# Kernel optimization log

Hardware: AMD Instinct MI355X
Metric: run time of the kernel (lower is better)

The kernel has to match this reference:

```python
import jax, jax.numpy as jnp
import numpy as np
from jax import lax

DN = ('NCDHW', 'OIDHW', 'NCDHW')

def conv3d(x, w, b, stride, pad):
    y = lax.conv_general_dilated(x, w, (stride,) * 3, [(pad, pad)] * 3,
                                 dimension_numbers=DN)
    return y + b[None, :, None, None, None]

def conv_transpose3d(x, w, b, stride=2, pad=1):
    # torch ConvTranspose3d weight layout: (Cin, Cout, k, k, k).
    # Equivalent conv: flip spatial dims, swap in/out, lhs_dilation=stride,
    # padding = k - 1 - pad.
    k = w.shape[2]
    wf = jnp.flip(w, (2, 3, 4)).transpose(1, 0, 2, 3, 4)
    p = k - 1 - pad
    y = lax.conv_general_dilated(x, wf, (1, 1, 1), [(p, p)] * 3,
                                 lhs_dilation=(stride,) * 3,
                                 dimension_numbers=DN)
    return y + b[None, :, None, None, None]

def setup_inputs() -> dict:
    key = jax.random.key(0)
    ks = jax.random.split(key, 20)
    B, C, S = 2, 3, 64
    CD, K = 256, 1024  # codebook_dim, codebook_size

    def w(k, shape):
        fan_in = int(np.prod(shape[1:]))
        return (jax.random.normal(k, shape, jnp.float32) / np.sqrt(fan_in)).astype(jnp.float32)

    inp = {"x": jax.random.normal(ks[0], (B, C, S, S, S), jnp.float32)}
    # encoder
    inp["enc_w1"] = w(ks[1], (64, C, 4, 4, 4));   inp["enc_b1"] = jnp.zeros((64,), jnp.float32)
    inp["enc_w2"] = w(ks[2], (128, 64, 4, 4, 4)); inp["enc_b2"] = jnp.zeros((128,), jnp.float32)
    inp["enc_w3"] = w(ks[3], (256, 128, 4, 4, 4)); inp["enc_b3"] = jnp.zeros((256,), jnp.float32)
    inp["enc_w4"] = w(ks[4], (CD, 256, 1, 1, 1)); inp["enc_b4"] = jnp.zeros((CD,), jnp.float32)
    # codebook (nn.Embedding weight)
    inp["codebook"] = jax.random.normal(ks[5], (K, CD), jnp.float32)
    # decoder (ConvTranspose weights in torch (Cin, Cout, k, k, k) layout)
    inp["dec_w1"] = w(ks[6], (CD, 256, 4, 4, 4)); inp["dec_b1"] = jnp.zeros((256,), jnp.float32)
    inp["dec_w2"] = w(ks[7], (256, 128, 4, 4, 4)); inp["dec_b2"] = jnp.zeros((128,), jnp.float32)
    inp["dec_w3"] = w(ks[8], (128, 64, 4, 4, 4)); inp["dec_b3"] = jnp.zeros((64,), jnp.float32)
    inp["dec_w4"] = w(ks[9], (C, 64, 4, 4, 4));   inp["dec_b4"] = jnp.zeros((C,), jnp.float32)
    return inp

def reference(x, enc_w1, enc_b1, enc_w2, enc_b2, enc_w3, enc_b3, enc_w4, enc_b4,
              codebook, dec_w1, dec_b1, dec_w2, dec_b2, dec_w3, dec_b3, dec_w4, dec_b4):
    # encoder
    h = jax.nn.relu(conv3d(x, enc_w1, enc_b1, 2, 1))
    h = jax.nn.relu(conv3d(h, enc_w2, enc_b2, 2, 1))
    h = jax.nn.relu(conv3d(h, enc_w3, enc_b3, 2, 1))
    latent = conv3d(h, enc_w4, enc_b4, 1, 0)  # (B, CD, H, W, D)
    B = latent.shape[0]
    H, W, D = latent.shape[2], latent.shape[3], latent.shape[4]
    CD = codebook.shape[1]
    # Faithful to torch: raw row-major .view(B, -1, CD) on channel-first latent
    lat = latent.reshape(B, -1, CD)  # (B, N, CD), N = H*W*D
    # argmin of L2 norm == argmin of squared distance (expand-norm trick,
    # avoids materializing the (B,N,K,CD) broadcast tensor)
    d2 = ((lat * lat).sum(-1, keepdims=True)
          - 2.0 * jnp.einsum('bnd,kd->bnk', lat, codebook)
          + (codebook * codebook).sum(-1)[None, None, :])  # (B, N, K)
    quantized_idx = jnp.argmin(d2, axis=-1)  # (B, N)
    quantized = codebook[quantized_idx]      # (B, N, CD)
    q = quantized.reshape(B, H, W, D, CD).transpose(0, 4, 1, 2, 3)  # (B, CD, H, W, D)
    # decoder
    h = jax.nn.relu(conv_transpose3d(q, dec_w1, dec_b1))
    h = jax.nn.relu(conv_transpose3d(h, dec_w2, dec_b2))
    h = jax.nn.relu(conv_transpose3d(h, dec_w3, dec_b3))
    reconstructed = jnp.tanh(conv3d(h, dec_w4, dec_b4, 1, 0))  # (B, C, S-3, S-3, S-3)
    return reconstructed, quantized_idx
```

## Files before the change

### kernel.cpp

```cpp
#include <hip/hip_runtime.h>
#include <cfloat>
#include <cmath>


using f32x4  = __attribute__((ext_vector_type(4))) float;
using bf16x8 = __attribute__((ext_vector_type(8))) short;
typedef float f32x4u __attribute__((ext_vector_type(4), aligned(4)));
typedef unsigned short u16x4u __attribute__((ext_vector_type(4), aligned(4)));
typedef unsigned short u16x8a4 __attribute__((ext_vector_type(8), aligned(4)));

__device__ __forceinline__ unsigned short f32_to_bf16(float f) {
    unsigned int u = __float_as_uint(f);
    u += 0x7fffu + ((u >> 16) & 1u);
    return (unsigned short)(u >> 16);
}
__device__ __forceinline__ void split_bf16(float v, unsigned short& h, unsigned short& l) {
    h = f32_to_bf16(v);
    float hf = __uint_as_float((unsigned)h << 16);
    l = f32_to_bf16(v - hf);
}
struct bf16t { unsigned short u; };
__device__ __forceinline__ void store_act(float* p, float v) { *p = v; }
__device__ __forceinline__ void store_act(unsigned short* p, float v) { *p = f32_to_bf16(v); }
__device__ __forceinline__ void store_act(bf16t* p, float v) {
    p->u = (unsigned short)(__float_as_uint(v) >> 16);
}

template <typename V>
__device__ __forceinline__ bf16x8 pack_b(V r0, V r1) {
    bf16x8 b;
    b[0] = (short)r0[0]; b[1] = (short)r0[1]; b[2] = (short)r0[2]; b[3] = (short)r0[3];
    b[4] = (short)r1[0]; b[5] = (short)r1[1]; b[6] = (short)r1[2]; b[7] = (short)r1[3];
    return b;
}

__global__ __launch_bounds__(256)
void prep_split_w(const float* __restrict__ w, short* __restrict__ whi,
                  short* __restrict__ wlo, long total)
{
    long idx = (long)blockIdx.x * blockDim.x + threadIdx.x;
    if (idx >= total) return;
    unsigned short h, l;
    split_bf16(w[idx], h, l);
    whi[idx] = (short)h; wlo[idx] = (short)l;
}

__global__ __launch_bounds__(256)
void prep_split_w_frag(const float* __restrict__ w, short* __restrict__ whi,
                       short* __restrict__ wlo, int CIN, int COUT)
{
    const int K = CIN * 64;
    const int MT = COUT >> 4;
    long total = (long)COUT * K;
    long idx = (long)blockIdx.x * blockDim.x + threadIdx.x;
    if (idx >= total) return;
    int kk = (int)(idx & 7); long r = idx >> 3;
    int l  = (int)(r & 63);  r >>= 6;
    int m  = (int)(r % MT);
    int s  = (int)(r / MT);
    int n16 = l & 15, quad = l >> 4;
    int co = m * 16 + n16;
    int korig = s * 32 + quad * 8 + kk;
    unsigned short h, lo16;
    split_bf16(w[(long)co * K + korig], h, lo16);
    whi[idx] = (short)h; wlo[idx] = (short)lo16;
}

__global__ __launch_bounds__(256)
void pad_input_split(const float* __restrict__ x, unsigned short* __restrict__ xhi,
                     unsigned short* __restrict__ xlo)
{
    const int D = 64, PD = 66, PRX = 68, BC = 6;
    long total = (long)BC * PD * PD * PRX;
    long idx = (long)blockIdx.x * blockDim.x + threadIdx.x;
    if (idx >= total) return;
    int px = (int)(idx % PRX); long t = idx / PRX;
    int py = (int)(t % PD); t /= PD;
    int pz = (int)(t % PD); int c = (int)(t / PD);
    int ix = px - 1, iy = py - 1, iz = pz - 1;
    float v = 0.0f;
    if ((unsigned)ix < (unsigned)D && (unsigned)iy < (unsigned)D && (unsigned)iz < (unsigned)D)
        v = x[(((long)c * D + iz) * D + iy) * D + ix];
    unsigned short h, l;
    split_bf16(v, h, l);
    xhi[idx] = h; xlo[idx] = l;
}

__global__ __launch_bounds__(256)
void zero_halo_ps(unsigned short* __restrict__ p, int C, int PD, int PRX)
{
    long total = (long)C * PD * PD * PRX;
    long idx = (long)blockIdx.x * blockDim.x + threadIdx.x;
    if (idx >= total) return;
    int px = (int)(idx % PRX); long t = idx / PRX;
    int py = (int)(t % PD); t /= PD;
    int pz = (int)(t % PD);
    if (px == 0 || px >= PD - 1 || py == 0 || py == PD - 1 || pz == 0 || pz == PD - 1)
        p[idx] = 0;
}

template <typename T>
__global__ __launch_bounds__(256) void zero_halo_t(T* __restrict__ p, int C, int PD)
{
    long total = (long)C * PD * PD * PD;
    long idx = (long)blockIdx.x * blockDim.x + threadIdx.x;
    if (idx >= total) return;
    int px = (int)(idx % PD); long t = idx / PD;
    int py = (int)(t % PD); t /= PD;
    int pz = (int)(t % PD);
    if (px == 0 || px == PD - 1 || py == 0 || py == PD - 1 || pz == 0 || pz == PD - 1)
        p[idx] = (T)0;
}

template <int CIN, int COUT, int DOUT, int PD, int PRX, int MTW, int OWT,
          int OWHALF, int KSPLIT, int OUTSPLIT>
__global__ __launch_bounds__(256)
void conv_s2_mfma(const unsigned short* __restrict__ xhi,
                  const unsigned short* __restrict__ xlo,
                  const short* __restrict__ Whi, const short* __restrict__ Wlo,
                  const float* __restrict__ bias,
                  unsigned short* __restrict__ yhi, unsigned short* __restrict__ ylo,
                  float* __restrict__ yf,
                  int OPD, int OPRX, int po, long sstride)
{
    constexpr int K = CIN * 64;
    constexpr int MWAVES = COUT / (16 * MTW);
    constexpr int RPB = 4 / MWAVES;
    constexpr int KN = (CIN * 2) / KSPLIT;

    int bx = blockIdx.x;
    const int ks = (KSPLIT > 1) ? (bx % KSPLIT) : 0;
    const int rowblk = (KSPLIT > 1) ? (bx / KSPLIT) : bx;
    const int lane = (int)threadIdx.x & 63, w = (int)threadIdx.x >> 6;
    const int mi = (MWAVES == 4) ? w : 0;
    const int ri = (MWAVES == 4) ? 0 : w;
    const int rowid = rowblk * RPB + ri;
    const int n16 = lane & 15, quad = lane >> 4;

    int b, od, oh, ow;
    if (OWHALF) {
        constexpr int NOH = DOUT / 2;
        const int ohb = rowid % NOH; int t = rowid / NOH;
        od = t % DOUT; b = t / DOUT;
        oh = ohb * 2 + (n16 >> 3);
        ow = n16 & 7;
    } else {
        const int owt = rowid % OWT; int t = rowid / OWT;
        oh = t % DOUT; t /= DOUT;
        od = t % DOUT; b = t / DOUT;
        ow = owt * 16 + n16;
    }

    const int co0 = mi * (MTW * 16);

    f32x4 acc[MTW];
    #pragma unroll
    for (int mt = 0; mt < MTW; ++mt)
        #pragma unroll
        for (int r = 0; r < 4; ++r) {
            int co = co0 + mt * 16 + quad * 4 + r;
            acc[mt][r] = (ks == 0) ? bias[co] : 0.0f;
        }

    const int sg0 = ks * KN;
    const long chs = (long)PD * PD * PRX;
    long off = ((long)(b * CIN + (sg0 >> 1)) * PD + (2 * od + (quad >> 1))) * PD * PRX
             + (long)(2 * oh + (quad & 1) * 2) * PRX + 2 * ow;
    const unsigned short* phi = xhi + off;
    const unsigned short* plo = xlo + off;
    const long incA = 2L * PD * PRX;
    const long incB = chs - 2L * PD * PRX;

    const short* a0h = Whi + (long)(co0 + n16) * K + sg0 * 32 + quad * 8;
    const short* a0l = Wlo + (long)(co0 + n16) * K + sg0 * 32 + quad * 8;

    #pragma unroll 2
    for (int s = 0; s < KN; ++s) {
        u16x4u h0 = *(const u16x4u*)phi;
        u16x4u h1 = *(const u16x4u*)(phi + PRX);
        u16x4u l0 = *(const u16x4u*)plo;
        u16x4u l1 = *(const u16x4u*)(plo + PRX);
        bf16x8 bhi = pack_b(h0, h1);
        bf16x8 blo = pack_b(l0, l1);
        #pragma unroll
        for (int mt = 0; mt < MTW; ++mt) {
            bf16x8 ah = *(const bf16x8*)(a0h + (long)mt * 16 * K + s * 32);
            bf16x8 al = *(const bf16x8*)(a0l + (long)mt * 16 * K + s * 32);
            acc[mt] = __builtin_amdgcn_mfma_f32_16x16x32_bf16(ah, bhi, acc[mt], 0, 0, 0);
            acc[mt] = __builtin_amdgcn_mfma_f32_16x16x32_bf16(ah, blo, acc[mt], 0, 0, 0);
            acc[mt] = __builtin_amdgcn_mfma_f32_16x16x32_bf16(al, bhi, acc[mt], 0, 0, 0);
        }
        long inc = (s & 1) ? incB : incA;
        phi += inc; plo += inc;
    }

    if (OUTSPLIT) {
        #pragma unroll
        for (int mt = 0; mt < MTW; ++mt)
            #pragma unroll
            for (int r = 0; r < 4; ++r) {
                int co = co0 + mt * 16 + quad * 4 + r;
                float v = fmaxf(acc[mt][r], 0.0f);
                unsigned short h, l;
                split_bf16(v, h, l);
                long o = (((long)(b * COUT + co) * OPD + od + po) * OPD + oh + po) * OPRX
                       + ow + po;
                yhi[o] = h; ylo[o] = l;
            }
    } else {
        #pragma unroll
        for (int mt = 0; mt < MTW; ++mt)
            #pragma unroll
            for (int r = 0; r < 4; ++r) {
                int co = co0 + mt * 16 + quad * 4 + r;
                long o = (long)ks * sstride
                       + (((long)(b * COUT + co) * OPD + od) * OPD + oh) * OPRX + ow;
                yf[o] = acc[mt][r];
            }
    }
}

template <int CIN, int COUT, int DOUT, int PD, int PRX, int MTW, int OWT,
          int OWHALF, int KSPLIT, int OUTSPLIT>
__global__ __launch_bounds__(256)
void conv_s2_mfma_fd(const unsigned short* __restrict__ xhi,
                     const unsigned short* __restrict__ xlo,
                     const short* __restrict__ Whi, const short* __restrict__ Wlo,
                     const float* __restrict__ bias,
                     unsigned short* __restrict__ yhi, unsigned short* __restrict__ ylo,
                     float* __restrict__ yf,
                     int OPD, int OPRX, int po, long sstride)
{
    constexpr int MWAVES = COUT / (16 * MTW);
    constexpr int RPB = 4 / MWAVES;
    constexpr int KN = (CIN * 2) / KSPLIT;
    constexpr int MT = COUT >> 4;
    constexpr int SSTEP = MT * 512;

    int bx = blockIdx.x;
    const int ks = (KSPLIT > 1) ? (bx % KSPLIT) : 0;
    const int rowblk = (KSPLIT > 1) ? (bx / KSPLIT) : bx;
    const int lane = (int)threadIdx.x & 63, w = (int)threadIdx.x >> 6;
    const int mi = (MWAVES == 4) ? w : 0;
    const int ri = (MWAVES == 4) ? 0 : w;
    const int rowid = rowblk * RPB + ri;
    const int n16 = lane & 15, quad = lane >> 4;

    int b, od, oh, ow;
    if (OWHALF) {
        constexpr int NOH = DOUT / 2;
        const int ohb = rowid % NOH; int t = rowid / NOH;
        od = t % DOUT; b = t / DOUT;
        oh = ohb * 2 + (n16 >> 3);
        ow = n16 & 7;
    } else {
        const int owt = rowid % OWT; int t = rowid / OWT;
        oh = t % DOUT; t /= DOUT;
        od = t % DOUT; b = t / DOUT;
        ow = owt * 16 + n16;
    }

    const int co0 = mi * (MTW * 16);

    f32x4 acc[MTW];
    #pragma unroll
    for (int mt = 0; mt < MTW; ++mt)
        #pragma unroll
        for (int r = 0; r < 4; ++r) {
            int co = co0 + mt * 16 + quad * 4 + r;
            acc[mt][r] = (ks == 0) ? bias[co] : 0.0f;
        }

    const int sg0 = ks * KN;
    const long chs = (long)PD * PD * PRX;
    long off = ((long)(b * CIN + (sg0 >> 1)) * PD + (2 * od + (quad >> 1))) * PD * PRX
             + (long)(2 * oh + (quad & 1) * 2) * PRX + 2 * ow;
    const unsigned short* phi = xhi + off;
    const unsigned short* plo = xlo + off;
    const long incA = 2L * PD * PRX;
    const long incB = chs - 2L * PD * PRX;

    const short* ph = Whi + (((long)sg0 * MT + mi * MTW) * 64 + lane) * 8;
    const short* pl = Wlo + (((long)sg0 * MT + mi * MTW) * 64 + lane) * 8;

    #pragma unroll 2
    for (int s = 0; s < KN; ++s) {
        u16x4u h0 = *(const u16x4u*)phi;
        u16x4u h1 = *(const u16x4u*)(phi + PRX);
        u16x4u l0 = *(const u16x4u*)plo;
        u16x4u l1 = *(const u16x4u*)(plo + PRX);
        bf16x8 bhi = pack_b(h0, h1);
        bf16x8 blo = pack_b(l0, l1);
        #pragma unroll
        for (int mt = 0; mt < MTW; ++mt) {
            bf16x8 ah = *(const bf16x8*)(ph + mt * 512);
            bf16x8 al = *(const bf16x8*)(pl + mt * 512);
            acc[mt] = __builtin_amdgcn_mfma_f32_16x16x32_bf16(ah, bhi, acc[mt], 0, 0, 0);
            acc[mt] = __builtin_amdgcn_mfma_f32_16x16x32_bf16(ah, blo, acc[mt], 0, 0, 0);
            acc[mt] = __builtin_amdgcn_mfma_f32_16x16x32_bf16(al, bhi, acc[mt], 0, 0, 0);
        }
        long inc = (s & 1) ? incB : incA;
        phi += inc; plo += inc;
        ph += SSTEP; pl += SSTEP;
    }

    if (OUTSPLIT) {
        #pragma unroll
        for (int mt = 0; mt < MTW; ++mt)
            #pragma unroll
            for (int r = 0; r < 4; ++r) {
                int co = co0 + mt * 16 + quad * 4 + r;
                float v = fmaxf(acc[mt][r], 0.0f);
                unsigned short h, l;
                split_bf16(v, h, l);
                long o = (((long)(b * COUT + co) * OPD + od + po) * OPD + oh + po) * OPRX
                       + ow + po;
                yhi[o] = h; ylo[o] = l;
            }
    } else {
        #pragma unroll
        for (int mt = 0; mt < MTW; ++mt)
            #pragma unroll
            for (int r = 0; r < 4; ++r) {
                int co = co0 + mt * 16 + quad * 4 + r;
                long o = (long)ks * sstride
                       + (((long)(b * COUT + co) * OPD + od) * OPD + oh) * OPRX + ow;
                yf[o] = acc[mt][r];
            }
    }
}

__global__ __launch_bounds__(256)
void combine4_relu(const float* __restrict__ p, float* __restrict__ y, long N, long ss)
{
    long idx = (long)blockIdx.x * blockDim.x + threadIdx.x;
    if (idx >= N) return;
    float v = p[idx] + p[idx + ss] + p[idx + 2 * ss] + p[idx + 3 * ss];
    y[idx] = fmaxf(v, 0.0f);
}

__global__ __launch_bounds__(128)
void conv1x1_b(const float* __restrict__ x, const float* __restrict__ w,
               const float* __restrict__ bias, float* __restrict__ y)
{
    const int co = blockIdx.x & 255, b = blockIdx.x >> 8;
    const int s4 = (int)threadIdx.x * 4;
    const float* xb = x + (long)b * 256 * 512 + s4;
    const float* wr = w + (long)co * 256;
    float bv = bias[co];
    float4 acc = {bv, bv, bv, bv};
    for (int ci = 0; ci < 256; ++ci) {
        float wv = wr[ci];
        float4 xv = *(const float4*)(xb + (long)ci * 512);
        acc.x = fmaf(xv.x, wv, acc.x); acc.y = fmaf(xv.y, wv, acc.y);
        acc.z = fmaf(xv.z, wv, acc.z); acc.w = fmaf(xv.w, wv, acc.w);
    }
    *(float4*)(y + (long)(b * 256 + co) * 512 + s4) = acc;
}

__global__ void codenorm_kernel(const float* __restrict__ cb, float* __restrict__ norms)
{
    int k = blockIdx.x;
    int lane = threadIdx.x;
    float s = 0.0f;
    const float* row = cb + (long)k * 256;
    for (int d = lane; d < 256; d += 64) { float v = row[d]; s = fmaf(v, v, s); }
    for (int off = 32; off > 0; off >>= 1) s += __shfl_down(s, off);
    if (lane == 0) norms[k] = s;
}

__global__ __launch_bounds__(256)
void transpose_cb(const float* __restrict__ cb, float* __restrict__ cbT)
{
    int idx = blockIdx.x * 256 + (int)threadIdx.x;
    int d = idx & 255, k = idx >> 8;
    cbT[(long)d * 1024 + k] = cb[(long)k * 256 + d];
}

__global__ __launch_bounds__(256)
void vq_kernel4(const float* __restrict__ lat, const float* __restrict__ cb,
                const float* __restrict__ cbT, const float* __restrict__ norms,
                unsigned short* __restrict__ q, float* __restrict__ idx_out)
{
    __shared__ __align__(16) float rows[4][256];
    __shared__ float s_best[4][256];
    __shared__ int   s_bidx[4][256];
    const int r0 = blockIdx.x * 4;
    const int t = (int)threadIdx.x;

    #pragma unroll
    for (int j = 0; j < 4; ++j)
        rows[j][t] = lat[(long)(r0 + j) * 256 + t];
    __syncthreads();

    float latn[4];
    #pragma unroll
    for (int j = 0; j < 4; ++j) {
        const float4* rowv = (const float4*)rows[j];
        float a = 0.0f;
        #pragma unroll 4
        for (int d = 0; d < 64; ++d) {
            float4 rv = rowv[d];
            a = fmaf(rv.x, rv.x, a); a = fmaf(rv.y, rv.y, a);
            a = fmaf(rv.z, rv.z, a); a = fmaf(rv.w, rv.w, a);
        }
        latn[j] = a;
    }

    float dot[4][4] = {};
    const float* ct = cbT + t * 4;
    #pragma unroll 4
    for (int d = 0; d < 256; ++d) {
        float4 c4 = *(const float4*)(ct + (long)d * 1024);
        #pragma unroll
        for (int j = 0; j < 4; ++j) {
            float rv = rows[j][d];
            dot[j][0] = fmaf(rv, c4.x, dot[j][0]);
            dot[j][1] = fmaf(rv, c4.y, dot[j][1]);
            dot[j][2] = fmaf(rv, c4.z, dot[j][2]);
            dot[j][3] = fmaf(rv, c4.w, dot[j][3]);
        }
    }

    float4 nv = *(const float4*)(norms + t * 4);
    float nr[4] = {nv.x, nv.y, nv.z, nv.w};

    #pragma unroll
    for (int j = 0; j < 4; ++j) {
        float best = FLT_MAX;
        int bidx = 0x7fffffff;
        #pragma unroll
        for (int c = 0; c < 4; ++c) {
            float sc = latn[j] - 2.0f * dot[j][c] + nr[c];
            int k = t * 4 + c;
            if (sc < best || (sc == best && k < bidx)) { best = sc; bidx = k; }
        }
        s_best[j][t] = best; s_bidx[j][t] = bidx;
    }
    __syncthreads();
    for (int off = 128; off > 0; off >>= 1) {
        if (t < off) {
            #pragma unroll
            for (int j = 0; j < 4; ++j) {
                float o = s_best[j][t + off]; int oi = s_bidx[j][t + off];
                if (o < s_best[j][t] || (o == s_best[j][t] && oi < s_bidx[j][t])) {
                    s_best[j][t] = o; s_bidx[j][t] = oi;
                }
            }
        }
        __syncthreads();
    }

    #pragma unroll
    for (int j = 0; j < 4; ++j) {
        const int bk = s_bidx[j][0];
        const int r = r0 + j;
        const int b = r >> 9, n = r & 511;
        const int zz = n >> 6, yy = (n >> 3) & 7, xx = n & 7;
        q[(long)(b * 256 + t) * 1000 + ((long)(zz + 1) * 10 + (yy + 1)) * 10 + (xx + 1)]
            = f32_to_bf16(cb[(long)bk * 256 + t]);
    }
    if (t == 0) {
        #pragma unroll
        for (int j = 0; j < 4; ++j)
            idx_out[r0 + j] = (float)s_bidx[j][0];
    }
}

__global__ __launch_bounds__(256)
void prep_convt_w(const float* __restrict__ w, short* __restrict__ Ap,
                  int Cin, int Cout, int xflip)
{
    const int K = Cin * 8;
    long total = 8L * Cout * K;
    long idx = (long)blockIdx.x * blockDim.x + threadIdx.x;
    if (idx >= total) return;
    int k = (int)(idx % K);
    int co = (int)((idx / K) % Cout);
    int p = (int)(idx / ((long)K * Cout));
    int ci = k >> 3, a = k & 7;
    int az = (a >> 2) & 1, ay = (a >> 1) & 1, ax = a & 1;
    int pz = p >> 2, py = (p >> 1) & 1, px = p & 1;
    int axw = xflip ? (1 - ax) : ax;
    int kd = (1 - pz) + 2 * az, kh = (1 - py) + 2 * ay, kw = (1 - px) + 2 * axw;
    float v = w[((long)ci * Cout + co) * 64 + kd * 16 + kh * 4 + kw];
    Ap[idx] = (short)f32_to_bf16(v);
}

__global__ __launch_bounds__(256)
void prep_convt_w_frag(const float* __restrict__ w, short* __restrict__ Ap,
                       int Cin, int Cout, int xflip)
{
    const int MG = Cout >> 6;
    const int nsteps = Cin >> 2;
    long total = 8L * MG * nsteps * 2048;
    long idx = (long)blockIdx.x * blockDim.x + threadIdx.x;
    if (idx >= total) return;
    int kk = (int)(idx & 7); long r = idx >> 3;
    int l  = (int)(r & 63);  r >>= 6;
    int cb = (int)(r & 3);   r >>= 2;
    int s  = (int)(r % nsteps); r /= nsteps;
    int mg = (int)(r % MG);
    int p  = (int)(r / MG);

    int n16 = l & 15, quad = l >> 4;
    int korig = s * 32 + quad * 8 + kk;
    int co = mg * 64 + cb * 16 + n16;
    int ci = korig >> 3, a = korig & 7;
    int az = (a >> 2) & 1, ay = (a >> 1) & 1, ax = a & 1;
    int pz = p >> 2, py = (p >> 1) & 1, px = p & 1;
    int axw = xflip ? (1 - ax) : ax;
    int kd = (1 - pz) + 2 * az, kh = (1 - py) + 2 * ay, kw = (1 - px) + 2 * axw;
    float v = w[((long)ci * Cout + co) * 64 + kd * 16 + kh * 4 + kw];
    Ap[idx] = (short)f32_to_bf16(v);
}

template <int CIN, int COUT, int DIN, int OPAD, typename OutT>
__global__ __launch_bounds__(256)
void convt_mfma(const unsigned short* __restrict__ Xp, const short* __restrict__ Ap,
                const float* __restrict__ bias, OutT* __restrict__ Y)
{
    constexpr int PD = DIN + 2;
    constexpr int PD3 = PD * PD * PD;
    constexpr int T = DIN >> 2;
    constexpr int NT = T * T * T;
    constexpr int SLAB = NT / 8;
    constexpr int OPD = 2 * DIN + 2 * OPAD;
    constexpr int K = CIN * 8;
    constexpr int MG = COUT >> 6;
    constexpr int nsteps = K >> 5;

    int bx = blockIdx.x;
    const int xcd = bx & 7;
    int local = bx >> 3;
    const int px = local & 1; local >>= 1;
    const int mg = local % MG; local /= MG;
    const int ntin = local % SLAB;
    const int pzy = local / SLAB;
    const int pz = pzy >> 1, py = pzy & 1;
    const int p = pz * 4 + py * 2 + px;
    const int nt = xcd * SLAB + ntin;

    const int lane = threadIdx.x & 63, wave = threadIdx.x >> 6;
    const int n16 = lane & 15, quad = lane >> 4;

    const int tx = nt % T, ty = (nt / T) % T, tz = nt / (T * T);
    const int mz = tz * 4 + wave, my = ty * 4 + (n16 >> 2), mx = tx * 4 + (n16 & 3);
    const int sp = ((mz + pz) * PD + (my + py)) * PD + (mx + px);

    const unsigned short* xq = Xp + (long)quad * PD3 + sp;

    const int cobase = mg * 64;
    const short* ap0 = Ap + ((long)p * COUT + cobase + n16) * K + quad * 8;

    f32x4 acc[4];
    #pragma unroll
    for (int cb = 0; cb < 4; ++cb) {
        const float* bp = bias + cobase + cb * 16 + quad * 4;
        acc[cb][0] = bp[0]; acc[cb][1] = bp[1]; acc[cb][2] = bp[2]; acc[cb][3] = bp[3];
    }

    #pragma unroll 4
    for (int s = 0; s < nsteps; ++s) {
        const unsigned short* xs = xq + (long)s * 4 * PD3;
        bf16x8 bf;
        bf[0] = (short)xs[(PD + 1) * PD + 1];
        bf[1] = (short)xs[(PD + 1) * PD];
        bf[2] = (short)xs[PD * PD + 1];
        bf[3] = (short)xs[PD * PD];
        bf[4] = (short)xs[PD + 1];
        bf[5] = (short)xs[PD];
        bf[6] = (short)xs[1];
        bf[7] = (short)xs[0];
        #pragma unroll
        for (int cb = 0; cb < 4; ++cb) {
            bf16x8 af = *(const bf16x8*)(ap0 + (long)cb * 16 * K + s * 32);
            acc[cb] = __builtin_amdgcn_mfma_f32_16x16x32_bf16(af, bf, acc[cb], 0, 0, 0);
        }
    }

    const int opz = 2 * mz + pz + OPAD, opy = 2 * my + py + OPAD, opx = 2 * mx + px + OPAD;
    const long spo = ((long)opz * OPD + opy) * OPD + opx;
    #pragma unroll
    for (int cb = 0; cb < 4; ++cb) {
        #pragma unroll
        for (int r = 0; r < 4; ++r) {
            int co = cobase + cb * 16 + quad * 4 + r;
            float v = fmaxf(acc[cb][r], 0.0f);
            store_act(Y + (long)co * OPD * OPD * OPD + spo, v);
        }
    }
}

template <int CIN, int COUT, int DIN, int OPAD, int MXP, int MYP, typename OutT>
__global__ __launch_bounds__(256)
void convt_mfma_v2(const unsigned short* __restrict__ Xp, const short* __restrict__ Ap,
                   const float* __restrict__ bias, OutT* __restrict__ Y)
{
    constexpr int PD = DIN + 2;
    constexpr int PD3 = PD * PD * PD;
    constexpr int OPD = 2 * DIN + 2 * OPAD;
    constexpr int K = CIN * 8;
    constexpr int MG = COUT >> 6;
    constexpr int nsteps = K >> 5;
    static_assert((nsteps & 1) == 0 && nsteps >= 4, "phase merge needs even nsteps");
    constexpr int NPH = nsteps / 2;
    constexpr int MXT = DIN / (16 * MXP);
    constexpr int MYT = DIN / (4 * MYP);
    constexpr int MZS = DIN / 8;
    constexpr int TPE = MXP * MYP;

    int bx = blockIdx.x;
    const int xcd = bx & 7;
    int local = bx >> 3;
    const int px = local & 1; local >>= 1;
    const int py = local & 1; local >>= 1;
    const int mg = local % MG; local /= MG;
    const int mxt = local % MXT; local /= MXT;
    const int myt = local % MYT; local /= MYT;
    const int pz = local & 1; local >>= 1;
    const int mzin = local;
    const int mz = xcd * MZS + mzin;
    const int p = pz * 4 + py * 2 + px;

    const int lane = threadIdx.x & 63, wave = threadIdx.x >> 6;
    const int n16 = lane & 15, quad = lane >> 4;

    const int mx0 = mxt * (16 * MXP) + n16;
    const int my0 = myt * (4 * MYP) + wave * MYP;
    const int baseX = mx0 & ~1;
    const int sh = 16 * ((n16 & 1) + px);
    const long sp = ((long)(mz + pz) * PD + (my0 + py)) * PD + baseX;

    const unsigned short* xq = Xp + (long)quad * PD3 + sp;

    const short* ApT = Ap + (((long)p * MG + mg) * nsteps) * 2048;

    __shared__ short Abuf[2][2][2048];

    f32x4 acc[TPE][4];
    #pragma unroll
    for (int t = 0; t < TPE; ++t)
        #pragma unroll
        for (int cb = 0; cb < 4; ++cb) {
            const float* bp = bias + (mg * 64) + cb * 16 + quad * 4;
            acc[t][cb][0] = bp[0]; acc[t][cb][1] = bp[1];
            acc[t][cb][2] = bp[2]; acc[t][cb][3] = bp[3];
        }

    constexpr int rowoff[4] = { (PD + 1) * PD, PD * PD, PD, 0 };
    union Frag { unsigned u[4]; bf16x8 b; };

    const int chunkoff = wave * 512 + lane * 8;

    {
        *(bf16x8*)(&Abuf[0][0][chunkoff]) = *(const bf16x8*)(ApT + chunkoff);
        *(bf16x8*)(&Abuf[0][1][chunkoff]) = *(const bf16x8*)(ApT + 2048 + chunkoff);
    }
    __syncthreads();

    #pragma unroll 1
    for (int ph = 0; ph < NPH; ++ph) {
        const int cur = ph & 1;
        const bool more = (ph + 1 < NPH);
        bf16x8 an0, an1;
        if (more) {
            an0 = *(const bf16x8*)(ApT + (long)(2 * ph + 2) * 2048 + chunkoff);
            an1 = *(const bf16x8*)(ApT + (long)(2 * ph + 3) * 2048 + chunkoff);
        }

        unsigned long long xr[2][TPE][4];
        #pragma unroll
        for (int u = 0; u < 2; ++u) {
            const unsigned short* xs = xq + (long)(2 * ph + u) * 4 * PD3;
            #pragma unroll
            for (int t = 0; t < TPE; ++t) {
                const int toff = (MXP > 1) ? t * 16 : t * PD;
                #pragma unroll
                for (int j = 0; j < 4; ++j) {
                    union { u16x4u v; unsigned long long u64; } ld;
                    ld.v = *(const u16x4u*)(xs + toff + rowoff[j]);
                    xr[u][t][j] = ld.u64;
                }
            }
        }

        bf16x8 af[2][4];
        #pragma unroll
        for (int u = 0; u < 2; ++u)
            #pragma unroll
            for (int cb = 0; cb < 4; ++cb)
                af[u][cb] = *(const bf16x8*)(&Abuf[cur][u][cb * 512 + lane * 8]);

        #pragma unroll
        for (int u = 0; u < 2; ++u) {
            #pragma unroll
            for (int t = 0; t < TPE; ++t) {
                Frag fr;
                #pragma unroll
                for (int j = 0; j < 4; ++j)
                    fr.u[j] = (unsigned)(xr[u][t][j] >> sh);
                #pragma unroll
                for (int cb = 0; cb < 4; ++cb)
                    acc[t][cb] = __builtin_amdgcn_mfma_f32_16x16x32_bf16(af[u][cb], fr.b,
                                                                         acc[t][cb], 0, 0, 0);
            }
        }

        if (more) {
            *(bf16x8*)(&Abuf[cur ^ 1][0][chunkoff]) = an0;
            *(bf16x8*)(&Abuf[cur ^ 1][1][chunkoff]) = an1;
        }
        __syncthreads();
    }

    const int opz = 2 * mz + pz + OPAD;
    #pragma unroll
    for (int t = 0; t < TPE; ++t) {
        const int opx = 2 * (mx0 + ((MXP > 1) ? t * 16 : 0)) + px + OPAD;
        const int opy = 2 * (my0 + ((MYP > 1) ? t : 0)) + py + OPAD;
        const long spo = ((long)opz * OPD + opy) * OPD + opx;
        #pragma unroll
        for (int cb = 0; cb < 4; ++cb) {
            #pragma unroll
            for (int r = 0; r < 4; ++r) {
                int co = (mg * 64) + cb * 16 + quad * 4 + r;
                float v = fmaxf(acc[t][cb][r], 0.0f);
                store_act(Y + (long)co * OPD * OPD * OPD + spo, v);
            }
        }
    }
}

__global__ __launch_bounds__(256)
void prep_dec4A_frag(const float* __restrict__ w, short* __restrict__ Aw)
{
    int idx = blockIdx.x * 256 + (int)threadIdx.x;
    int kk = idx & 7;
    int l  = (idx >> 3) & 63;
    int s  = idx >> 9;
    int n16 = l & 15, quad = l >> 4;
    int k = s * 32 + quad * 8 + kk;
    float v = (n16 < 3) ? w[n16 * 4096 + k] : 0.0f;
    Aw[idx] = (short)f32_to_bf16(v);
}

__global__ __launch_bounds__(256)
void conv_dec4_mfma(const unsigned short* __restrict__ d3h, const short* __restrict__ Aw,
                    const float* __restrict__ bias, float* __restrict__ y)
{
    constexpr int D = 64, Dout = 61;
    constexpr int RS = 80;
    int bx = blockIdx.x;
    const int slab = bx & 7;
    const int i = bx >> 3;
    const int od = slab * 8 + (i >> 4);
    const int oh0 = (i & 15) * 4;
    if (od >= Dout) return;
    const int tid = (int)threadIdx.x;
    const int lane = tid & 63, wave = tid >> 6;
    const int n16 = lane & 15, quad = lane >> 4;
    const int ow = wave * 16 + n16;

    __shared__ unsigned short Xs[2][28][RS];
    unsigned short* xsb = &Xs[0][0][0];
    constexpr int BUFW = 28 * RS;

    f32x4 acc[4];
    #pragma unroll
    for (int j = 0; j < 4; ++j)
        #pragma unroll
        for (int r = 0; r < 4; ++r) {
            int co = quad * 4 + r;
            acc[j][r] = (co < 3) ? bias[co] : 0.0f;
        }

    const int kd0 = quad >> 1;
    const int kh0 = (quad & 1) * 2;
    const int sha = 16 * (ow & 1);
    const int owb = ow & ~1;

    const bool sact = (tid < 224);
    int goff[8];
    int loff[8];
    #pragma unroll
    for (int j = 0; j < 8; ++j) {
        const int g = tid + 224 * j;
        const int row = g >> 6, xx = g & 63;
        const int szi = row / 7, syi = row % 7;
        goff[j] = ((od + szi) * D + min(oh0 + syi, D - 1)) * D + xx;
        loff[j] = row * RS + xx;
    }
    auto choff = [](int S) { return (long)S * D * D * D; };

    if (sact) {
        #pragma unroll
        for (int j = 0; j < 8; ++j)
            xsb[loff[j]] = d3h[goff[j]];
    }
    __syncthreads();

    #pragma unroll 1
    for (int S = 0; S < 64; ++S) {
        const int cur = S & 1;
        const bool more = (S + 1 < 64);
        unsigned short nv[8];
        if (more && sact) {
            const unsigned short* src = d3h + choff(S + 1);
            #pragma unroll
            for (int j = 0; j < 8; ++j)
                nv[j] = src[goff[j]];
        }

        #pragma unroll
        for (int h = 0; h < 2; ++h) {
            bf16x8 af = *(const bf16x8*)(Aw + ((long)(2 * S + h) * 64 + lane) * 8);
            unsigned p0[5], p1[5];
            #pragma unroll
            for (int r = 0; r < 5; ++r) {
                const int row = 14 * h + kd0 * 7 + kh0 + r;
                union { u16x8a4 v; unsigned long long q[2]; } ld;
                ld.v = *(const u16x8a4*)(xsb + cur * BUFW + row * RS + owb);
                p0[r] = (unsigned)(ld.q[0] >> sha);
                p1[r] = (unsigned)(((ld.q[0] >> 32) | (ld.q[1] << 32)) >> sha);
            }
            #pragma unroll
            for (int j = 0; j < 4; ++j) {
                union { unsigned u[4]; bf16x8 b; } fr;
                fr.u[0] = p0[j];     fr.u[1] = p1[j];
                fr.u[2] = p0[j + 1]; fr.u[3] = p1[j + 1];
                acc[j] = __builtin_amdgcn_mfma_f32_16x16x32_bf16(af, fr.b, acc[j], 0, 0, 0);
            }
        }

        if (more && sact) {
            unsigned short* dst = xsb + (cur ^ 1) * BUFW;
            #pragma unroll
            for (int j = 0; j < 8; ++j)
                dst[loff[j]] = nv[j];
        }
        __syncthreads();
    }

    if (ow < Dout && quad == 0) {
        #pragma unroll
        for (int j = 0; j < 4; ++j) {
            const int oh = oh0 + j;
            if (oh >= Dout) continue;
            #pragma unroll
            for (int r = 0; r < 3; ++r)
                y[((long)(r * Dout + od) * Dout + oh) * Dout + ow] = tanhf(acc[j][r]);
        }
    }
}

extern "C" void kernel_launch(void* const* d_in, const int* in_sizes, int n_in,
                              void* d_out, int out_size, void* d_ws, size_t ws_size,
                              hipStream_t stream)
{
    const float* x        = (const float*)d_in[0];
    const float* enc_w1   = (const float*)d_in[1];
    const float* enc_b1   = (const float*)d_in[2];
    const float* enc_w2   = (const float*)d_in[3];
    const float* enc_b2   = (const float*)d_in[4];
    const float* enc_w3   = (const float*)d_in[5];
    const float* enc_b3   = (const float*)d_in[6];
    const float* enc_w4   = (const float*)d_in[7];
    const float* enc_b4   = (const float*)d_in[8];
    const float* codebook = (const float*)d_in[9];
    const float* dec_w1   = (const float*)d_in[10];
    const float* dec_b1   = (const float*)d_in[11];
    const float* dec_w2   = (const float*)d_in[12];
    const float* dec_b2   = (const float*)d_in[13];
    const float* dec_w3   = (const float*)d_in[14];
    const float* dec_b3   = (const float*)d_in[15];
    const float* dec_w4   = (const float*)d_in[16];
    const float* dec_b4   = (const float*)d_in[17];

    float* out = (float*)d_out;
    float* idx_out = out + 2L * 3 * 61 * 61 * 61;

    char* wsb = (char*)d_ws;
    float*          cn   = (float*)wsb;
    unsigned short* qp   = (unsigned short*)(wsb + 4096);
    short*          Ap1  = (short*)(wsb + 1028096);
    short*          Ap2  = (short*)(wsb + 9416704);
    short*          Ap3  = (short*)(wsb + 13611008);
    short*          Aw4  = (short*)(wsb + 14659584);
    short*          W1hi = (short*)(wsb + 14790656);
    short*          W1lo = (short*)(wsb + 14815232);
    short*          W2hi = (short*)(wsb + 14839808);
    short*          W2lo = (short*)(wsb + 15888384);
    short*          W3hi = (short*)(wsb + 16936960);
    short*          W3lo = (short*)(wsb + 21131264);
    char* arena = wsb + 25325568;
    unsigned short* xphi = (unsigned short*)arena;
    unsigned short* xplo = (unsigned short*)(arena + 3554496);
    unsigned short* h1hi = (unsigned short*)(arena + 7108992);
    unsigned short* h1lo = (unsigned short*)(arena + 17762688);
    unsigned short* h2hi = (unsigned short*)(arena + 28416384);
    unsigned short* h2lo = (unsigned short*)(arena + 31734144);
    float*          pp3  = (float*)(arena + 35051904);
    float*          h3   = (float*)(arena + 39246208);
    float*          lat  = (float*)(arena + 40294784);
    unsigned short* d1 = (unsigned short*)arena;
    unsigned short* d2 = (unsigned short*)(arena + 2985984);
    bf16t*          d3 = (bf16t*)(arena + 13047808);
    float*          cbT = (float*)(wsb + 105482240);

    dim3 blk(256);
    auto nblk = [](long n) { return dim3((unsigned)((n + 255) / 256)); };

    prep_convt_w<<<nblk(8L * 256 * 2048), blk, 0, stream>>>(dec_w1, Ap1, 256, 256, 0);
    prep_convt_w_frag<<<nblk(8L * 128 * 2048), blk, 0, stream>>>(dec_w2, Ap2, 256, 128, 1);
    prep_convt_w_frag<<<nblk(8L * 64 * 1024), blk, 0, stream>>>(dec_w3, Ap3, 128, 64, 1);
    prep_dec4A_frag<<<dim3(256), blk, 0, stream>>>(dec_w4, Aw4);
    prep_split_w<<<nblk(12288), blk, 0, stream>>>(enc_w1, W1hi, W1lo, 12288);
    prep_split_w_frag<<<nblk(524288), blk, 0, stream>>>(enc_w2, W2hi, W2lo, 64, 128);
    prep_split_w_frag<<<nblk(2097152), blk, 0, stream>>>(enc_w3, W3hi, W3lo, 128, 256);
    transpose_cb<<<dim3(1024), blk, 0, stream>>>(codebook, cbT);

    pad_input_split<<<nblk(6L * 66 * 66 * 68), blk, 0, stream>>>(x, xphi, xplo);
    zero_halo_ps<<<nblk(128L * 34 * 34 * 36), blk, 0, stream>>>(h1hi, 128, 34, 36);
    zero_halo_ps<<<nblk(128L * 34 * 34 * 36), blk, 0, stream>>>(h1lo, 128, 34, 36);
    conv_s2_mfma<3, 64, 32, 66, 68, 4, 2, 0, 1, 1><<<dim3(1024), blk, 0, stream>>>(
        xphi, xplo, W1hi, W1lo, enc_b1, h1hi, h1lo, nullptr, 34, 36, 1, 0);
    zero_halo_ps<<<nblk(256L * 18 * 18 * 20), blk, 0, stream>>>(h2hi, 256, 18, 20);
    zero_halo_ps<<<nblk(256L * 18 * 18 * 20), blk, 0, stream>>>(h2lo, 256, 18, 20);
    conv_s2_mfma_fd<64, 128, 16, 34, 36, 2, 1, 0, 1, 1><<<dim3(512), blk, 0, stream>>>(
        h1hi, h1lo, W2hi, W2lo, enc_b2, h2hi, h2lo, nullptr, 18, 20, 1, 0);
    conv_s2_mfma_fd<128, 256, 8, 18, 20, 4, 1, 1, 4, 0><<<dim3(256), blk, 0, stream>>>(
        h2hi, h2lo, W3hi, W3lo, enc_b3, nullptr, nullptr, pp3, 8, 8, 0, 262144);
    combine4_relu<<<nblk(262144), blk, 0, stream>>>(pp3, h3, 262144, 262144);
    conv1x1_b<<<dim3(512), dim3(128), 0, stream>>>(h3, enc_w4, enc_b4, lat);

    codenorm_kernel<<<dim3(1024), dim3(64), 0, stream>>>(codebook, cn);
    zero_halo_t<unsigned short><<<nblk(512L * 10 * 10 * 10), blk, 0, stream>>>(qp, 512, 10);
    vq_kernel4<<<dim3(256), blk, 0, stream>>>(lat, codebook, cbT, cn, qp, idx_out);

    zero_halo_t<unsigned short><<<nblk(256L * 18 * 18 * 18), blk, 0, stream>>>(d1, 256, 18);
    zero_halo_t<unsigned short><<<nblk(128L * 34 * 34 * 34), blk, 0, stream>>>(d2, 128, 34);

    for (int b = 0; b < 2; ++b) {
        const unsigned short* qb = qp + (long)b * 256 * 1000;
        float* outb = out + (long)b * 3 * 226981;
        convt_mfma<256, 256, 8, 1, unsigned short><<<dim3(256), blk, 0, stream>>>(
            qb, Ap1, dec_b1, d1);
        convt_mfma_v2<256, 128, 16, 1, 1, 2, unsigned short><<<dim3(512), blk, 0, stream>>>(
            d1, Ap2, dec_b2, d2);
        convt_mfma_v2<128, 64, 32, 0, 2, 1, bf16t><<<dim3(2048), blk, 0, stream>>>(
            d2, Ap3, dec_b3, d3);
        conv_dec4_mfma<<<dim3(8 * 8 * 16), blk, 0, stream>>>(
            (const unsigned short*)d3, Aw4, dec_b4, outb);
    }
}
```

Baseline: 886.0 us.

## Store decoder intermediate d2 in channel-interleaved-by-4 layout for vectorized access

Changes the d2 activation between the second and third transposed convolutions from planar channel-major to a layout that interleaves groups of 4 channels per spatial site. The producer writes 4 channels with one 8-byte store instead of 4 scattered 2-byte stores, and the consumer loads 16-byte vectors and extracts each lane's channel by shifting. A matching halo-zeroing kernel is added. The intent is fewer, wider memory transactions. The cost is extra bit manipulation in the consumer, and the 16-byte loads fetch two spatial sites where the consumer may only need one column.

```diff
diff --git a/kernel.cpp b/kernel.cpp
--- a/kernel.cpp
+++ b/kernel.cpp
@@ -112,6 +112,21 @@
         p[idx] = (T)0;
 }
 
+__global__ __launch_bounds__(256)
+void zero_halo_i4(unsigned short* __restrict__ p, int CG, int PD)
+{
+    long pd3 = (long)PD * PD * PD;
+    long total = (long)CG * pd3 * 4;
+    long idx = (long)blockIdx.x * blockDim.x + threadIdx.x;
+    if (idx >= total) return;
+    long sp = (idx >> 2) % pd3;
+    int px = (int)(sp % PD); long t = sp / PD;
+    int py = (int)(t % PD);
+    int pz = (int)(t / PD);
+    if (px == 0 || px == PD - 1 || py == 0 || py == PD - 1 || pz == 0 || pz == PD - 1)
+        p[idx] = 0;
+}
+
 template <int CIN, int COUT, int DOUT, int PD, int PRX, int MTW, int OWT,
           int OWHALF, int KSPLIT, int OUTSPLIT>
 __global__ __launch_bounds__(256)
@@ -592,7 +607,8 @@
     }
 }
 
-template <int CIN, int COUT, int DIN, int OPAD, int MXP, int MYP, typename OutT>
+template <int CIN, int COUT, int DIN, int OPAD, int MXP, int MYP, int IIN, int IOUT,
+          typename OutT>
 __global__ __launch_bounds__(256)
 void convt_mfma_v2(const unsigned short* __restrict__ Xp, const short* __restrict__ Ap,
                    const float* __restrict__ bias, OutT* __restrict__ Y)
@@ -630,9 +646,11 @@
     const int my0 = myt * (4 * MYP) + wave * MYP;
     const int baseX = mx0 & ~1;
     const int sh = 16 * ((n16 & 1) + px);
-    const long sp = ((long)(mz + pz) * PD + (my0 + py)) * PD + baseX;
-
-    const unsigned short* xq = Xp + (long)quad * PD3 + sp;
+    const int shq = 16 * quad;
+
+    const long spLin = ((long)(mz + pz) * PD + (my0 + py)) * PD + baseX;
+    const long spInt = ((long)(mz + pz) * PD + (my0 + py)) * PD + mx0 + px;
+    const unsigned short* xq = IIN ? Xp : (Xp + (long)quad * PD3 + spLin);
 
     const short* ApT = Ap + (((long)p * MG + mg) * nsteps) * 2048;
 
@@ -670,17 +688,24 @@
         }
 
         unsigned long long xr[2][TPE][4];
+        u16x8a4 raw16[2][TPE][4];
         #pragma unroll
         for (int u = 0; u < 2; ++u) {
-            const unsigned short* xs = xq + (long)(2 * ph + u) * 4 * PD3;
+            const int s = 2 * ph + u;
             #pragma unroll
             for (int t = 0; t < TPE; ++t) {
                 const int toff = (MXP > 1) ? t * 16 : t * PD;
                 #pragma unroll
                 for (int j = 0; j < 4; ++j) {
-                    union { u16x4u v; unsigned long long u64; } ld;
-                    ld.v = *(const u16x4u*)(xs + toff + rowoff[j]);
-                    xr[u][t][j] = ld.u64;
+                    if constexpr (IIN) {
+                        raw16[u][t][j] = *(const u16x8a4*)(
+                            Xp + ((long)s * PD3 + spInt + toff + rowoff[j]) * 4);
+                    } else {
+                        const unsigned short* xs = xq + (long)s * 4 * PD3;
+                        union { u16x4u v; unsigned long long u64; } ld;
+                        ld.v = *(const u16x4u*)(xs + toff + rowoff[j]);
+                        xr[u][t][j] = ld.u64;
+                    }
                 }
             }
         }
@@ -698,8 +723,17 @@
             for (int t = 0; t < TPE; ++t) {
                 Frag fr;
                 #pragma unroll
-                for (int j = 0; j < 4; ++j)
-                    fr.u[j] = (unsigned)(xr[u][t][j] >> sh);
+                for (int j = 0; j < 4; ++j) {
+                    if constexpr (IIN) {
+                        union { u16x8a4 v; unsigned long long q[2]; } c;
+                        c.v = raw16[u][t][j];
+                        unsigned lo = (unsigned)((c.q[0] >> shq) & 0xffffULL);
+                        unsigned hi = (unsigned)((c.q[1] >> shq) & 0xffffULL);
+                        fr.u[j] = lo | (hi << 16);
+                    } else {
+                        fr.u[j] = (unsigned)(xr[u][t][j] >> sh);
+                    }
+                }
                 #pragma unroll
                 for (int cb = 0; cb < 4; ++cb)
                     acc[t][cb] = __builtin_amdgcn_mfma_f32_16x16x32_bf16(af[u][cb], fr.b,
@@ -722,11 +756,20 @@
         const long spo = ((long)opz * OPD + opy) * OPD + opx;
         #pragma unroll
         for (int cb = 0; cb < 4; ++cb) {
-            #pragma unroll
-            for (int r = 0; r < 4; ++r) {
-                int co = (mg * 64) + cb * 16 + quad * 4 + r;
-                float v = fmaxf(acc[t][cb][r], 0.0f);
-                store_act(Y + (long)co * OPD * OPD * OPD + spo, v);
+            if constexpr (IOUT) {
+                const int cg = mg * 16 + cb * 4 + quad;
+                u16x4u st;
+                #pragma unroll
+                for (int r = 0; r < 4; ++r)
+                    st[r] = f32_to_bf16(fmaxf(acc[t][cb][r], 0.0f));
+                *(u16x4u*)((unsigned short*)Y + ((long)cg * OPD * OPD * OPD + spo) * 4) = st;
+            } else {
+                #pragma unroll
+                for (int r = 0; r < 4; ++r) {
+                    int co = (mg * 64) + cb * 16 + quad * 4 + r;
+                    float v = fmaxf(acc[t][cb][r], 0.0f);
+                    store_act(Y + (long)co * OPD * OPD * OPD + spo, v);
+                }
             }
         }
     }
@@ -939,17 +982,17 @@
     vq_kernel4<<<dim3(256), blk, 0, stream>>>(lat, codebook, cbT, cn, qp, idx_out);
 
     zero_halo_t<unsigned short><<<nblk(256L * 18 * 18 * 18), blk, 0, stream>>>(d1, 256, 18);
-    zero_halo_t<unsigned short><<<nblk(128L * 34 * 34 * 34), blk, 0, stream>>>(d2, 128, 34);
+    zero_halo_i4<<<nblk(128L * 34 * 34 * 34), blk, 0, stream>>>(d2, 32, 34);
 
     for (int b = 0; b < 2; ++b) {
         const unsigned short* qb = qp + (long)b * 256 * 1000;
         float* outb = out + (long)b * 3 * 226981;
         convt_mfma<256, 256, 8, 1, unsigned short><<<dim3(256), blk, 0, stream>>>(
             qb, Ap1, dec_b1, d1);
-        convt_mfma_v2<256, 128, 16, 1, 1, 2, unsigned short><<<dim3(512), blk, 0, stream>>>(
-            d1, Ap2, dec_b2, d2);
-        convt_mfma_v2<128, 64, 32, 0, 2, 1, bf16t><<<dim3(2048), blk, 0, stream>>>(
-            d2, Ap3, dec_b3, d3);
+        convt_mfma_v2<256, 128, 16, 1, 1, 2, 0, 1, unsigned short>
+            <<<dim3(512), blk, 0, stream>>>(d1, Ap2, dec_b2, d2);
+        convt_mfma_v2<128, 64, 32, 0, 2, 1, 1, 0, bf16t>
+            <<<dim3(2048), blk, 0, stream>>>(d2, Ap3, dec_b3, d3);
         conv_dec4_mfma<<<dim3(8 * 8 * 16), blk, 0, stream>>>(
             (const unsigned short*)d3, Aw4, dec_b4, outb);
     }
```

Measured after the change: 893.7 us. About the same (+0.9%).
